# Performance work log

Hardware: AMD Instinct MI355X
Metric: run time of the kernel (lower is better)

The kernel has to match this reference:

```python
import jax, jax.numpy as jnp
import numpy as np

NODE_DIM = 512
PROMPT_DIM = 512
N_NODES = 100000
N_GRAPHS = 1024


def setup_inputs() -> dict:
    key = jax.random.key(0)
    k1, k2, k3, k4, k5, k6, k7 = jax.random.split(key, 7)
    node_feats = jax.random.normal(k1, (N_NODES, NODE_DIM), dtype=jnp.float32)
    graph_prompt = jax.random.normal(k2, (N_GRAPHS, PROMPT_DIM), dtype=jnp.float32)
    batch_idx = jnp.sort(jax.random.randint(k3, (N_NODES,), 0, N_GRAPHS))
    # Linear init ~ U(-1/sqrt(fan_in), 1/sqrt(fan_in)) like torch defaults
    fan1 = NODE_DIM + PROMPT_DIM
    b1 = 1.0 / np.sqrt(fan1)
    W1 = jax.random.uniform(k4, (fan1, NODE_DIM), minval=-b1, maxval=b1, dtype=jnp.float32)
    bias1 = jax.random.uniform(k5, (NODE_DIM,), minval=-b1, maxval=b1, dtype=jnp.float32)
    b2 = 1.0 / np.sqrt(NODE_DIM)
    W2 = jax.random.uniform(k6, (NODE_DIM, NODE_DIM), minval=-b2, maxval=b2, dtype=jnp.float32)
    bias2 = jax.random.uniform(k7, (NODE_DIM,), minval=-b2, maxval=b2, dtype=jnp.float32)
    return {"node_feats": node_feats, "graph_prompt": graph_prompt, "batch_idx": batch_idx,
            "W1": W1, "bias1": bias1, "W2": W2, "bias2": bias2}


def reference(node_feats, graph_prompt, batch_idx, W1, bias1, W2, bias2):
    # gather per-node prompt: [N, prompt_dim]
    prompt_expanded = graph_prompt[batch_idx]
    combined = jnp.concatenate([node_feats, prompt_expanded], axis=-1)  # [N, node_dim+prompt_dim]
    h = jax.nn.relu(combined @ W1 + bias1)  # [N, node_dim]
    return h @ W2 + bias2  # [N, node_dim]
```

## Files before the change

kernel.cpp:

```cpp
#include <hip/hip_runtime.h>


#define N_NODES 100000
#define NWG 3128

typedef __bf16 bf16x8 __attribute__((ext_vector_type(8)));
typedef float  f32x4  __attribute__((ext_vector_type(4)));
typedef unsigned short ushort_t;

__device__ __forceinline__ ushort_t f2bf(float f) {
  __bf16 b = (__bf16)f;
  return __builtin_bit_cast(unsigned short, b);
}

__device__ __forceinline__ bf16x8 cvt8(const float* p) {
  float4 x = *(const float4*)p;
  float4 y = *(const float4*)(p + 4);
  bf16x8 v;
  v[0] = (__bf16)x.x; v[1] = (__bf16)x.y; v[2] = (__bf16)x.z; v[3] = (__bf16)x.w;
  v[4] = (__bf16)y.x; v[5] = (__bf16)y.y; v[6] = (__bf16)y.z; v[7] = (__bf16)y.w;
  return v;
}

__device__ __forceinline__ bf16x8 cvt8v(float4 x, float4 y) {
  bf16x8 v;
  v[0] = (__bf16)x.x; v[1] = (__bf16)x.y; v[2] = (__bf16)x.z; v[3] = (__bf16)x.w;
  v[4] = (__bf16)y.x; v[5] = (__bf16)y.y; v[6] = (__bf16)y.z; v[7] = (__bf16)y.w;
  return v;
}

__device__ __forceinline__ void gload_lds16(const void* g, void* l) {
  __builtin_amdgcn_global_load_lds(
      (const __attribute__((address_space(1))) void*)g,
      (__attribute__((address_space(3))) void*)l, 16, 0, 0);
}

__global__ void prep_kernel(const float* __restrict__ W1, const float* __restrict__ W2,
                            ushort_t* __restrict__ W1T, ushort_t* __restrict__ W2T) {
  int i = blockIdx.x * 256 + threadIdx.x;
  if (i < 524288) {
    int n = i >> 10, k = i & 1023;
    W1T[i] = f2bf(W1[k * 512 + n]);
  } else if (i < 786432) {
    int j = i - 524288;
    int n = j >> 9, k = j & 511;
    W2T[j] = f2bf(W2[k * 512 + n]);
  }
}

__global__ __launch_bounds__(256, 4) void p2_kernel(
    const float* __restrict__ gp, const ushort_t* __restrict__ W1T,
    const float* __restrict__ bias1, float* __restrict__ P2) {
  const int tid = threadIdx.x, lane = tid & 63, wid = tid >> 6;
  const int lc = lane & 15, lr = lane >> 4;
  const int m0 = (blockIdx.x >> 1) * 32;
  const int col0 = (blockIdx.x & 1) * 256 + wid * 64;

  f32x4 acc[2][4];
#pragma unroll
  for (int i = 0; i < 2; ++i)
#pragma unroll
    for (int j = 0; j < 4; ++j) acc[i][j] = {0.f, 0.f, 0.f, 0.f};

  const float* a0 = gp + (size_t)(m0 + lc) * 512;
  const ushort_t* bb = W1T + (size_t)(col0 + lc) * 1024 + 512;

#pragma unroll 2
  for (int kt = 0; kt < 8; ++kt) {
    bf16x8 bfr[2][4];
#pragma unroll
    for (int kk = 0; kk < 2; ++kk)
#pragma unroll
      for (int j = 0; j < 4; ++j)
        bfr[kk][j] = *(const bf16x8*)(bb + (size_t)j * 16 * 1024 + kt * 64 + kk * 32 + lr * 8);
    bf16x8 af[2][2];
#pragma unroll
    for (int i = 0; i < 2; ++i)
#pragma unroll
      for (int kk = 0; kk < 2; ++kk)
        af[i][kk] = cvt8(a0 + (size_t)i * 16 * 512 + kt * 64 + kk * 32 + lr * 8);
#pragma unroll
    for (int kk = 0; kk < 2; ++kk)
#pragma unroll
      for (int i = 0; i < 2; ++i)
#pragma unroll
        for (int j = 0; j < 4; ++j)
          acc[i][j] = __builtin_amdgcn_mfma_f32_16x16x32_bf16(af[i][kk], bfr[kk][j], acc[i][j], 0, 0, 0);
  }

#pragma unroll
  for (int i = 0; i < 2; ++i)
#pragma unroll
    for (int r = 0; r < 4; ++r) {
      int row = m0 + i * 16 + lr * 4 + r;
#pragma unroll
      for (int j = 0; j < 4; ++j) {
        int col = col0 + j * 16 + lc;
        P2[(size_t)row * 512 + col] = acc[i][j][r] + bias1[col];
      }
    }
}

__global__ __launch_bounds__(256, 4) void g1_kernel(
    const float* __restrict__ nf, const int* __restrict__ bidx,
    const ushort_t* __restrict__ W1T, const float* __restrict__ P2,
    ushort_t* __restrict__ h) {
  __shared__ ushort_t sA[128 * 64];
  __shared__ ushort_t sB[128 * 64];

  const int tid = threadIdx.x, lane = tid & 63, wid = tid >> 6;
  const int tile = (blockIdx.x & 7) * 391 + (blockIdx.x >> 3);
  const int m0 = (tile >> 2) * 128, n0 = (tile & 3) * 128;

  const float* pAg[4]; int ldsA[4];
#pragma unroll
  for (int s = 0; s < 4; ++s) {
    int q = s * 256 + tid;
    int row = q >> 3;
    int cw = (q & 7) ^ (row & 7);
    int rowg = m0 + row; if (rowg > N_NODES - 1) rowg = N_NODES - 1;
    pAg[s] = nf + (size_t)rowg * 512 + cw * 8;
    ldsA[s] = q * 8;
  }
  const ushort_t* pB[4]; int ldsB[4];
#pragma unroll
  for (int s = 0; s < 4; ++s) {
    int q = wid * 256 + s * 64 + lane;
    int row = q >> 3;
    int cw = (q & 7) ^ (row & 7);
    pB[s] = W1T + (size_t)(n0 + row) * 1024 + cw * 8;
    ldsB[s] = (wid * 256 + s * 64) * 8;
  }

  f32x4 acc[4][4];
#pragma unroll
  for (int i = 0; i < 4; ++i)
#pragma unroll
    for (int j = 0; j < 4; ++j) acc[i][j] = {0.f, 0.f, 0.f, 0.f};

  const int wm = (wid >> 1) * 64, wn = (wid & 1) * 64;
  const int lr = lane >> 4, lc = lane & 15;

  for (int kt = 0; kt < 8; ++kt) {
    float4 ax[4], ay[4];
#pragma unroll
    for (int s = 0; s < 4; ++s) {
      ax[s] = *(const float4*)(pAg[s]);
      ay[s] = *(const float4*)(pAg[s] + 4);
      pAg[s] += 64;
    }
#pragma unroll
    for (int s = 0; s < 4; ++s) { gload_lds16(pB[s], &sB[ldsB[s]]); pB[s] += 64; }
#pragma unroll
    for (int s = 0; s < 4; ++s)
      *(bf16x8*)&sA[ldsA[s]] = cvt8v(ax[s], ay[s]);
    __syncthreads();

#pragma unroll
    for (int kk = 0; kk < 2; ++kk) {
      bf16x8 af[4], bfr[4];
#pragma unroll
      for (int i = 0; i < 4; ++i) {
        int row = wm + i * 16 + lc;
        int cp = (kk * 4 + lr) ^ (row & 7);
        af[i] = *(const bf16x8*)&sA[row * 64 + cp * 8];
      }
#pragma unroll
      for (int j = 0; j < 4; ++j) {
        int col = wn + j * 16 + lc;
        int cp = (kk * 4 + lr) ^ (col & 7);
        bfr[j] = *(const bf16x8*)&sB[col * 64 + cp * 8];
      }
#pragma unroll
      for (int i = 0; i < 4; ++i)
#pragma unroll
        for (int j = 0; j < 4; ++j)
          acc[i][j] = __builtin_amdgcn_mfma_f32_16x16x32_bf16(af[i], bfr[j], acc[i][j], 0, 0, 0);
    }
    __syncthreads();
  }

#pragma unroll
  for (int i = 0; i < 4; ++i) {
#pragma unroll
    for (int r = 0; r < 4; ++r) {
      int row = m0 + wm + i * 16 + lr * 4 + r;
      if (row < N_NODES) {
        int g = bidx[row];
        const float* p2r = P2 + (size_t)g * 512 + n0 + wn;
#pragma unroll
        for (int j = 0; j < 4; ++j) {
          float v = fmaxf(acc[i][j][r] + p2r[j * 16 + lc], 0.f);
          h[(size_t)row * 512 + n0 + wn + j * 16 + lc] = f2bf(v);
        }
      }
    }
  }
}

__global__ __launch_bounds__(256, 4) void g2_kernel(
    const ushort_t* __restrict__ h, const ushort_t* __restrict__ W2T,
    const float* __restrict__ bias2, float* __restrict__ out) {
  __shared__ ushort_t sA[128 * 64];
  __shared__ ushort_t sB[128 * 64];

  const int tid = threadIdx.x, lane = tid & 63, wid = tid >> 6;
  const int tile = (blockIdx.x & 7) * 391 + (blockIdx.x >> 3);
  const int m0 = (tile >> 2) * 128, n0 = (tile & 3) * 128;

  const ushort_t* pA[4]; const ushort_t* pB[4]; int ldsW[4];
#pragma unroll
  for (int s = 0; s < 4; ++s) {
    int q = wid * 256 + s * 64 + lane;
    int row = q >> 3;
    int cw = (q & 7) ^ (row & 7);
    int rowg = m0 + row; if (rowg > N_NODES - 1) rowg = N_NODES - 1;
    pA[s] = h + (size_t)rowg * 512 + cw * 8;
    pB[s] = W2T + (size_t)(n0 + row) * 512 + cw * 8;
    ldsW[s] = (wid * 256 + s * 64) * 8;
  }

  f32x4 acc[4][4];
#pragma unroll
  for (int i = 0; i < 4; ++i)
#pragma unroll
    for (int j = 0; j < 4; ++j) acc[i][j] = {0.f, 0.f, 0.f, 0.f};

  const int wm = (wid >> 1) * 64, wn = (wid & 1) * 64;
  const int lr = lane >> 4, lc = lane & 15;

  for (int kt = 0; kt < 8; ++kt) {
#pragma unroll
    for (int s = 0; s < 4; ++s) {
      gload_lds16(pA[s], &sA[ldsW[s]]); pA[s] += 64;
      gload_lds16(pB[s], &sB[ldsW[s]]); pB[s] += 64;
    }
    __syncthreads();
#pragma unroll
    for (int kk = 0; kk < 2; ++kk) {
      bf16x8 af[4], bfr[4];
#pragma unroll
      for (int i = 0; i < 4; ++i) {
        int row = wm + i * 16 + lc;
        int cp = (kk * 4 + lr) ^ (row & 7);
        af[i] = *(const bf16x8*)&sA[row * 64 + cp * 8];
      }
#pragma unroll
      for (int j = 0; j < 4; ++j) {
        int col = wn + j * 16 + lc;
        int cp = (kk * 4 + lr) ^ (col & 7);
        bfr[j] = *(const bf16x8*)&sB[col * 64 + cp * 8];
      }
#pragma unroll
      for (int i = 0; i < 4; ++i)
#pragma unroll
        for (int j = 0; j < 4; ++j)
          acc[i][j] = __builtin_amdgcn_mfma_f32_16x16x32_bf16(af[i], bfr[j], acc[i][j], 0, 0, 0);
    }
    __syncthreads();
  }

#pragma unroll
  for (int j = 0; j < 4; ++j) {
    int col = n0 + wn + j * 16 + lc;
    float bv = bias2[col];
#pragma unroll
    for (int i = 0; i < 4; ++i)
#pragma unroll
      for (int r = 0; r < 4; ++r) {
        int row = m0 + wm + i * 16 + lr * 4 + r;
        if (row < N_NODES) out[(size_t)row * 512 + col] = acc[i][j][r] + bv;
      }
  }
}

extern "C" void kernel_launch(void* const* d_in, const int* in_sizes, int n_in,
                              void* d_out, int out_size, void* d_ws, size_t ws_size,
                              hipStream_t stream) {
  const float* nf   = (const float*)d_in[0];
  const float* gp   = (const float*)d_in[1];
  const int*   bidx = (const int*)d_in[2];
  const float* W1   = (const float*)d_in[3];
  const float* b1   = (const float*)d_in[4];
  const float* W2   = (const float*)d_in[5];
  const float* b2   = (const float*)d_in[6];
  float* out = (float*)d_out;

  char* ws = (char*)d_ws;
  ushort_t* W1T = (ushort_t*)ws;
  ushort_t* W2T = (ushort_t*)(ws + 1048576);
  float*    P2  = (float*)   (ws + 1572864);
  ushort_t* hbf = (ushort_t*)(ws + 3670016);

  prep_kernel<<<3072, 256, 0, stream>>>(W1, W2, W1T, W2T);
  p2_kernel<<<64, 256, 0, stream>>>(gp, W1T, b1, P2);
  g1_kernel<<<NWG, 256, 0, stream>>>(nf, bidx, W1T, P2, hbf);
  g2_kernel<<<NWG, 256, 0, stream>>>(hbf, W2T, b2, out);
}
```

Baseline: 276.5 us.

## Double-buffer LDS tiles in both GEMM kernels to overlap loads with MFMA

Both GEMM kernels now use two LDS buffers for A and B. Each iteration prefetches the next K-slice into the alternate buffer while the current one is being computed, so one barrier per iteration replaces two. This should hide global-load latency behind MFMA work. In exchange, LDS use doubles to 64KB per block and the launch bound drops from 4 to 2 blocks per CU, which may reduce the occupancy-based latency hiding the kernels had before.

```diff
diff --git a/kernel.cpp b/kernel.cpp
--- a/kernel.cpp
+++ b/kernel.cpp
@@ -101,12 +101,12 @@
     }
 }
 
-__global__ __launch_bounds__(256, 4) void g1_kernel(
+__global__ __launch_bounds__(256, 2) void g1_kernel(
     const float* __restrict__ nf, const int* __restrict__ bidx,
     const ushort_t* __restrict__ W1T, const float* __restrict__ P2,
     ushort_t* __restrict__ h) {
-  __shared__ ushort_t sA[128 * 64];
-  __shared__ ushort_t sB[128 * 64];
+  __shared__ ushort_t sA[2][128 * 64];
+  __shared__ ushort_t sB[2][128 * 64];
 
   const int tid = threadIdx.x, lane = tid & 63, wid = tid >> 6;
   const int tile = (blockIdx.x & 7) * 391 + (blockIdx.x >> 3);
@@ -141,7 +141,7 @@
   const int wm = (wid >> 1) * 64, wn = (wid & 1) * 64;
   const int lr = lane >> 4, lc = lane & 15;
 
-  for (int kt = 0; kt < 8; ++kt) {
+  {
     float4 ax[4], ay[4];
 #pragma unroll
     for (int s = 0; s < 4; ++s) {
@@ -150,12 +150,28 @@
       pAg[s] += 64;
     }
 #pragma unroll
-    for (int s = 0; s < 4; ++s) { gload_lds16(pB[s], &sB[ldsB[s]]); pB[s] += 64; }
-#pragma unroll
-    for (int s = 0; s < 4; ++s)
-      *(bf16x8*)&sA[ldsA[s]] = cvt8v(ax[s], ay[s]);
+    for (int s = 0; s < 4; ++s) { gload_lds16(pB[s], &sB[0][ldsB[s]]); pB[s] += 64; }
+#pragma unroll
+    for (int s = 0; s < 4; ++s) *(bf16x8*)&sA[0][ldsA[s]] = cvt8v(ax[s], ay[s]);
     __syncthreads();
-
+  }
+
+#pragma unroll
+  for (int kt = 0; kt < 8; ++kt) {
+    const int cur = kt & 1;
+    float4 ax[4], ay[4];
+    if (kt < 7) {
+#pragma unroll
+      for (int s = 0; s < 4; ++s) {
+        ax[s] = *(const float4*)(pAg[s]);
+        ay[s] = *(const float4*)(pAg[s] + 4);
+        pAg[s] += 64;
+      }
+#pragma unroll
+      for (int s = 0; s < 4; ++s) {
+        gload_lds16(pB[s], &sB[cur ^ 1][ldsB[s]]); pB[s] += 64;
+      }
+    }
 #pragma unroll
     for (int kk = 0; kk < 2; ++kk) {
       bf16x8 af[4], bfr[4];
@@ -163,13 +179,13 @@
       for (int i = 0; i < 4; ++i) {
         int row = wm + i * 16 + lc;
         int cp = (kk * 4 + lr) ^ (row & 7);
-        af[i] = *(const bf16x8*)&sA[row * 64 + cp * 8];
+        af[i] = *(const bf16x8*)&sA[cur][row * 64 + cp * 8];
       }
 #pragma unroll
       for (int j = 0; j < 4; ++j) {
         int col = wn + j * 16 + lc;
         int cp = (kk * 4 + lr) ^ (col & 7);
-        bfr[j] = *(const bf16x8*)&sB[col * 64 + cp * 8];
+        bfr[j] = *(const bf16x8*)&sB[cur][col * 64 + cp * 8];
       }
 #pragma unroll
       for (int i = 0; i < 4; ++i)
@@ -177,7 +193,12 @@
         for (int j = 0; j < 4; ++j)
           acc[i][j] = __builtin_amdgcn_mfma_f32_16x16x32_bf16(af[i], bfr[j], acc[i][j], 0, 0, 0);
     }
-    __syncthreads();
+    if (kt < 7) {
+#pragma unroll
+      for (int s = 0; s < 4; ++s)
+        *(bf16x8*)&sA[cur ^ 1][ldsA[s]] = cvt8v(ax[s], ay[s]);
+      __syncthreads();
+    }
   }
 
 #pragma unroll
@@ -198,11 +219,11 @@
   }
 }
 
-__global__ __launch_bounds__(256, 4) void g2_kernel(
+__global__ __launch_bounds__(256, 2) void g2_kernel(
     const ushort_t* __restrict__ h, const ushort_t* __restrict__ W2T,
     const float* __restrict__ bias2, float* __restrict__ out) {
-  __shared__ ushort_t sA[128 * 64];
-  __shared__ ushort_t sB[128 * 64];
+  __shared__ ushort_t sA[2][128 * 64];
+  __shared__ ushort_t sB[2][128 * 64];
 
   const int tid = threadIdx.x, lane = tid & 63, wid = tid >> 6;
   const int tile = (blockIdx.x & 7) * 391 + (blockIdx.x >> 3);
@@ -229,13 +250,23 @@
   const int wm = (wid >> 1) * 64, wn = (wid & 1) * 64;
   const int lr = lane >> 4, lc = lane & 15;
 
+#pragma unroll
+  for (int s = 0; s < 4; ++s) {
+    gload_lds16(pA[s], &sA[0][ldsW[s]]); pA[s] += 64;
+    gload_lds16(pB[s], &sB[0][ldsW[s]]); pB[s] += 64;
+  }
+  __syncthreads();
+
+#pragma unroll
   for (int kt = 0; kt < 8; ++kt) {
-#pragma unroll
-    for (int s = 0; s < 4; ++s) {
-      gload_lds16(pA[s], &sA[ldsW[s]]); pA[s] += 64;
-      gload_lds16(pB[s], &sB[ldsW[s]]); pB[s] += 64;
-    }
-    __syncthreads();
+    const int cur = kt & 1;
+    if (kt < 7) {
+#pragma unroll
+      for (int s = 0; s < 4; ++s) {
+        gload_lds16(pA[s], &sA[cur ^ 1][ldsW[s]]); pA[s] += 64;
+        gload_lds16(pB[s], &sB[cur ^ 1][ldsW[s]]); pB[s] += 64;
+      }
+    }
 #pragma unroll
     for (int kk = 0; kk < 2; ++kk) {
       bf16x8 af[4], bfr[4];
@@ -243,13 +274,13 @@
       for (int i = 0; i < 4; ++i) {
         int row = wm + i * 16 + lc;
         int cp = (kk * 4 + lr) ^ (row & 7);
-        af[i] = *(const bf16x8*)&sA[row * 64 + cp * 8];
+        af[i] = *(const bf16x8*)&sA[cur][row * 64 + cp * 8];
       }
 #pragma unroll
       for (int j = 0; j < 4; ++j) {
         int col = wn + j * 16 + lc;
         int cp = (kk * 4 + lr) ^ (col & 7);
-        bfr[j] = *(const bf16x8*)&sB[col * 64 + cp * 8];
+        bfr[j] = *(const bf16x8*)&sB[cur][col * 64 + cp * 8];
       }
 #pragma unroll
       for (int i = 0; i < 4; ++i)
@@ -257,7 +288,7 @@
         for (int j = 0; j < 4; ++j)
           acc[i][j] = __builtin_amdgcn_mfma_f32_16x16x32_bf16(af[i], bfr[j], acc[i][j], 0, 0, 0);
     }
-    __syncthreads();
+    if (kt < 7) __syncthreads();
   }
 
 #pragma unroll
```

Measured after the change: 344.6 us. +24.6%, slower.

## Register-prefetch pipeline GEMMs, two M tiles per workgroup, XCD-contiguous tile mapping

Applied to the files above, without the earlier changes.

Both GEMM kernels now prefetch the next K slice into registers while MFMAs run on the current LDS tile. This replaces the global_load_lds DMA path with plain loads followed by LDS stores between barriers. Each workgroup processes two consecutive 128-row tiles, so the grid is halved and the prologue is amortised. A new XCD mapping keeps neighbouring tiles on the same XCD, and setprio is raised around the MFMA section. Occupancy bounds drop to 2 waves per SIMD to make room for the extra prefetch registers, at the cost of less latency hiding across workgroups.

```diff
diff --git a/kernel.cpp b/kernel.cpp
--- a/kernel.cpp
+++ b/kernel.cpp
@@ -2,7 +2,7 @@
 
 
 #define N_NODES 100000
-#define NWG 3128
+#define NWG 1564
 
 typedef __bf16 bf16x8 __attribute__((ext_vector_type(8)));
 typedef float  f32x4  __attribute__((ext_vector_type(4)));
@@ -29,10 +29,15 @@
   return v;
 }
 
-__device__ __forceinline__ void gload_lds16(const void* g, void* l) {
-  __builtin_amdgcn_global_load_lds(
-      (const __attribute__((address_space(1))) void*)g,
-      (__attribute__((address_space(3))) void*)l, 16, 0, 0);
+__device__ __forceinline__ void block_sync() {
+  __builtin_amdgcn_sched_barrier(0);
+  __builtin_amdgcn_s_barrier();
+  __builtin_amdgcn_sched_barrier(0);
+}
+
+__device__ __forceinline__ int xcd_map(int b) {
+  int xcd = b & 7, pos = b >> 3;
+  return (xcd < 4 ? xcd * 196 : 784 + (xcd - 4) * 195) + pos;
 }
 
 __global__ void prep_kernel(const float* __restrict__ W1, const float* __restrict__ W2,
@@ -101,7 +106,7 @@
     }
 }
 
-__global__ __launch_bounds__(256, 4) void g1_kernel(
+__global__ __launch_bounds__(256, 2) void g1_kernel(
     const float* __restrict__ nf, const int* __restrict__ bidx,
     const ushort_t* __restrict__ W1T, const float* __restrict__ P2,
     ushort_t* __restrict__ h) {
@@ -109,27 +114,25 @@
   __shared__ ushort_t sB[128 * 64];
 
   const int tid = threadIdx.x, lane = tid & 63, wid = tid >> 6;
-  const int tile = (blockIdx.x & 7) * 391 + (blockIdx.x >> 3);
-  const int m0 = (tile >> 2) * 128, n0 = (tile & 3) * 128;
-
-  const float* pAg[4]; int ldsA[4];
+  const int wg = xcd_map(blockIdx.x);
+  const int group = wg >> 2, nt = wg & 3;
+  const int m0 = group * 256;
+  const int n0 = nt * 128;
+
+  int arow[4], acw[4];
+  const float* pAg[4];
+  const ushort_t* pB[4];
+  int ldsQ[4];
 #pragma unroll
   for (int s = 0; s < 4; ++s) {
     int q = s * 256 + tid;
     int row = q >> 3;
     int cw = (q & 7) ^ (row & 7);
+    arow[s] = row; acw[s] = cw;
     int rowg = m0 + row; if (rowg > N_NODES - 1) rowg = N_NODES - 1;
     pAg[s] = nf + (size_t)rowg * 512 + cw * 8;
-    ldsA[s] = q * 8;
-  }
-  const ushort_t* pB[4]; int ldsB[4];
-#pragma unroll
-  for (int s = 0; s < 4; ++s) {
-    int q = wid * 256 + s * 64 + lane;
-    int row = q >> 3;
-    int cw = (q & 7) ^ (row & 7);
-    pB[s] = W1T + (size_t)(n0 + row) * 1024 + cw * 8;
-    ldsB[s] = (wid * 256 + s * 64) * 8;
+    pB[s]  = W1T + (size_t)(n0 + row) * 1024 + cw * 8;
+    ldsQ[s] = q * 8;
   }
 
   f32x4 acc[4][4];
@@ -141,21 +144,44 @@
   const int wm = (wid >> 1) * 64, wn = (wid & 1) * 64;
   const int lr = lane >> 4, lc = lane & 15;
 
-  for (int kt = 0; kt < 8; ++kt) {
-    float4 ax[4], ay[4];
+  {
+    float4 ax[4], ay[4]; int4 bv[4];
 #pragma unroll
     for (int s = 0; s < 4; ++s) {
       ax[s] = *(const float4*)(pAg[s]);
       ay[s] = *(const float4*)(pAg[s] + 4);
-      pAg[s] += 64;
-    }
-#pragma unroll
-    for (int s = 0; s < 4; ++s) { gload_lds16(pB[s], &sB[ldsB[s]]); pB[s] += 64; }
-#pragma unroll
-    for (int s = 0; s < 4; ++s)
-      *(bf16x8*)&sA[ldsA[s]] = cvt8v(ax[s], ay[s]);
+      bv[s] = *(const int4*)(pB[s]);
+      pAg[s] += 64; pB[s] += 64;
+    }
+#pragma unroll
+    for (int s = 0; s < 4; ++s) {
+      *(bf16x8*)&sA[ldsQ[s]] = cvt8v(ax[s], ay[s]);
+      *(int4*)&sB[ldsQ[s]] = bv[s];
+    }
     __syncthreads();
-
+  }
+
+  float4 ax[4], ay[4]; int4 bvr[4];
+#pragma unroll
+  for (int s = 0; s < 16; ++s) {
+    if (s < 15) {
+      if (s == 7) {
+#pragma unroll
+        for (int t = 0; t < 4; ++t) {
+          int rowg = m0 + 128 + arow[t]; if (rowg > N_NODES - 1) rowg = N_NODES - 1;
+          pAg[t] = nf + (size_t)rowg * 512 + acw[t] * 8;
+          pB[t] -= 512;
+        }
+      }
+#pragma unroll
+      for (int t = 0; t < 4; ++t) {
+        ax[t] = *(const float4*)(pAg[t]);
+        ay[t] = *(const float4*)(pAg[t] + 4);
+        bvr[t] = *(const int4*)(pB[t]);
+        pAg[t] += 64; pB[t] += 64;
+      }
+    }
+    __builtin_amdgcn_s_setprio(1);
 #pragma unroll
     for (int kk = 0; kk < 2; ++kk) {
       bf16x8 af[4], bfr[4];
@@ -177,65 +203,124 @@
         for (int j = 0; j < 4; ++j)
           acc[i][j] = __builtin_amdgcn_mfma_f32_16x16x32_bf16(af[i], bfr[j], acc[i][j], 0, 0, 0);
     }
-    __syncthreads();
-  }
-
-#pragma unroll
-  for (int i = 0; i < 4; ++i) {
-#pragma unroll
-    for (int r = 0; r < 4; ++r) {
-      int row = m0 + wm + i * 16 + lr * 4 + r;
-      if (row < N_NODES) {
-        int g = bidx[row];
-        const float* p2r = P2 + (size_t)g * 512 + n0 + wn;
-#pragma unroll
-        for (int j = 0; j < 4; ++j) {
-          float v = fmaxf(acc[i][j][r] + p2r[j * 16 + lc], 0.f);
-          h[(size_t)row * 512 + n0 + wn + j * 16 + lc] = f2bf(v);
+    __builtin_amdgcn_s_setprio(0);
+
+    if (s < 15) {
+      block_sync();
+#pragma unroll
+      for (int t = 0; t < 4; ++t) {
+        *(bf16x8*)&sA[ldsQ[t]] = cvt8v(ax[t], ay[t]);
+        *(int4*)&sB[ldsQ[t]] = bvr[t];
+      }
+      asm volatile("s_waitcnt lgkmcnt(0)" ::: "memory");
+      block_sync();
+    }
+
+    if (s == 7 || s == 15) {
+      const int m0t = m0 + (s >> 3) * 128;
+#pragma unroll
+      for (int i = 0; i < 4; ++i) {
+#pragma unroll
+        for (int r = 0; r < 4; ++r) {
+          int row = m0t + wm + i * 16 + lr * 4 + r;
+          if (row < N_NODES) {
+            int g = bidx[row];
+            const float* p2r = P2 + (size_t)g * 512 + n0 + wn;
+#pragma unroll
+            for (int j = 0; j < 4; ++j) {
+              float v = fmaxf(acc[i][j][r] + p2r[j * 16 + lc], 0.f);
+              h[(size_t)row * 512 + n0 + wn + j * 16 + lc] = f2bf(v);
+            }
+          }
         }
       }
-    }
-  }
-}
-
-__global__ __launch_bounds__(256, 4) void g2_kernel(
+      if (s == 7) {
+#pragma unroll
+        for (int i = 0; i < 4; ++i)
+#pragma unroll
+          for (int j = 0; j < 4; ++j) acc[i][j] = {0.f, 0.f, 0.f, 0.f};
+      }
+    }
+  }
+}
+
+__global__ __launch_bounds__(256, 2) void g2_kernel(
     const ushort_t* __restrict__ h, const ushort_t* __restrict__ W2T,
     const float* __restrict__ bias2, float* __restrict__ out) {
   __shared__ ushort_t sA[128 * 64];
   __shared__ ushort_t sB[128 * 64];
 
   const int tid = threadIdx.x, lane = tid & 63, wid = tid >> 6;
-  const int tile = (blockIdx.x & 7) * 391 + (blockIdx.x >> 3);
-  const int m0 = (tile >> 2) * 128, n0 = (tile & 3) * 128;
-
-  const ushort_t* pA[4]; const ushort_t* pB[4]; int ldsW[4];
+  const int wg = xcd_map(blockIdx.x);
+  const int group = wg >> 2, nt = wg & 3;
+  const int m0 = group * 256;
+  const int n0 = nt * 128;
+
+  int arow[4], acw[4];
+  const ushort_t* pA[4];
+  const ushort_t* pB[4];
+  int ldsQ[4];
 #pragma unroll
   for (int s = 0; s < 4; ++s) {
-    int q = wid * 256 + s * 64 + lane;
+    int q = s * 256 + tid;
     int row = q >> 3;
     int cw = (q & 7) ^ (row & 7);
+    arow[s] = row; acw[s] = cw;
     int rowg = m0 + row; if (rowg > N_NODES - 1) rowg = N_NODES - 1;
     pA[s] = h + (size_t)rowg * 512 + cw * 8;
     pB[s] = W2T + (size_t)(n0 + row) * 512 + cw * 8;
-    ldsW[s] = (wid * 256 + s * 64) * 8;
-  }
-
-  f32x4 acc[4][4];
-#pragma unroll
-  for (int i = 0; i < 4; ++i)
-#pragma unroll
-    for (int j = 0; j < 4; ++j) acc[i][j] = {0.f, 0.f, 0.f, 0.f};
+    ldsQ[s] = q * 8;
+  }
 
   const int wm = (wid >> 1) * 64, wn = (wid & 1) * 64;
   const int lr = lane >> 4, lc = lane & 15;
 
-  for (int kt = 0; kt < 8; ++kt) {
+  float bv2[4];
+#pragma unroll
+  for (int j = 0; j < 4; ++j) bv2[j] = bias2[n0 + wn + j * 16 + lc];
+
+  f32x4 acc[4][4];
+#pragma unroll
+  for (int i = 0; i < 4; ++i)
+#pragma unroll
+    for (int j = 0; j < 4; ++j) acc[i][j] = {0.f, 0.f, 0.f, 0.f};
+
+  {
+    int4 av[4], bv[4];
 #pragma unroll
     for (int s = 0; s < 4; ++s) {
-      gload_lds16(pA[s], &sA[ldsW[s]]); pA[s] += 64;
-      gload_lds16(pB[s], &sB[ldsW[s]]); pB[s] += 64;
+      av[s] = *(const int4*)(pA[s]);
+      bv[s] = *(const int4*)(pB[s]);
+      pA[s] += 64; pB[s] += 64;
+    }
+#pragma unroll
+    for (int s = 0; s < 4; ++s) {
+      *(int4*)&sA[ldsQ[s]] = av[s];
+      *(int4*)&sB[ldsQ[s]] = bv[s];
     }
     __syncthreads();
+  }
+
+  int4 avr[4], bvr[4];
+#pragma unroll
+  for (int s = 0; s < 16; ++s) {
+    if (s < 15) {
+      if (s == 7) {
+#pragma unroll
+        for (int t = 0; t < 4; ++t) {
+          int rowg = m0 + 128 + arow[t]; if (rowg > N_NODES - 1) rowg = N_NODES - 1;
+          pA[t] = h + (size_t)rowg * 512 + acw[t] * 8;
+          pB[t] -= 512;
+        }
+      }
+#pragma unroll
+      for (int t = 0; t < 4; ++t) {
+        avr[t] = *(const int4*)(pA[t]);
+        bvr[t] = *(const int4*)(pB[t]);
+        pA[t] += 64; pB[t] += 64;
+      }
+    }
+    __builtin_amdgcn_s_setprio(1);
 #pragma unroll
     for (int kk = 0; kk < 2; ++kk) {
       bf16x8 af[4], bfr[4];
@@ -257,20 +342,39 @@
         for (int j = 0; j < 4; ++j)
           acc[i][j] = __builtin_amdgcn_mfma_f32_16x16x32_bf16(af[i], bfr[j], acc[i][j], 0, 0, 0);
     }
-    __syncthreads();
-  }
-
-#pragma unroll
-  for (int j = 0; j < 4; ++j) {
-    int col = n0 + wn + j * 16 + lc;
-    float bv = bias2[col];
-#pragma unroll
-    for (int i = 0; i < 4; ++i)
-#pragma unroll
-      for (int r = 0; r < 4; ++r) {
-        int row = m0 + wm + i * 16 + lr * 4 + r;
-        if (row < N_NODES) out[(size_t)row * 512 + col] = acc[i][j][r] + bv;
-      }
+    __builtin_amdgcn_s_setprio(0);
+
+    if (s < 15) {
+      block_sync();
+#pragma unroll
+      for (int t = 0; t < 4; ++t) {
+        *(int4*)&sA[ldsQ[t]] = avr[t];
+        *(int4*)&sB[ldsQ[t]] = bvr[t];
+      }
+      asm volatile("s_waitcnt lgkmcnt(0)" ::: "memory");
+      block_sync();
+    }
+
+    if (s == 7 || s == 15) {
+      const int m0t = m0 + (s >> 3) * 128;
+#pragma unroll
+      for (int j = 0; j < 4; ++j) {
+        int col = n0 + wn + j * 16 + lc;
+#pragma unroll
+        for (int i = 0; i < 4; ++i)
+#pragma unroll
+          for (int r = 0; r < 4; ++r) {
+            int row = m0t + wm + i * 16 + lr * 4 + r;
+            if (row < N_NODES) out[(size_t)row * 512 + col] = acc[i][j][r] + bv2[j];
+          }
+      }
+      if (s == 7) {
+#pragma unroll
+        for (int i = 0; i < 4; ++i)
+#pragma unroll
+          for (int j = 0; j < 4; ++j) acc[i][j] = {0.f, 0.f, 0.f, 0.f};
+      }
+    }
   }
 }
 
```

Measured after the change: 589.6 us. 113% more time.

## Software-pipeline A-tile register prefetch in both GEMM kernels with manual waitcnt

Applied to the files above, without the earlier changes.

Both GEMM kernels now prefetch the next K-slice of the A operand into registers while the current slice is being consumed. In g2 the A tile moves from direct global-to-LDS loads to a register-staged path, and the loops are fully unrolled. __syncthreads is replaced by explicit s_waitcnt with partial vmcnt counts plus raw s_barrier and sched_barrier, so the next A loads stay in flight across the MFMA phase. This aims to hide global load latency behind compute, at the cost of more registers and a hand-tuned vmcnt count that must match the issued load order.

```diff
diff --git a/kernel.cpp b/kernel.cpp
--- a/kernel.cpp
+++ b/kernel.cpp
@@ -141,20 +141,34 @@
   const int wm = (wid >> 1) * 64, wn = (wid & 1) * 64;
   const int lr = lane >> 4, lc = lane & 15;
 
+  float4 ax[4], ay[4];
+#pragma unroll
+  for (int s = 0; s < 4; ++s) {
+    ax[s] = *(const float4*)(pAg[s]);
+    ay[s] = *(const float4*)(pAg[s] + 4);
+    pAg[s] += 64;
+  }
+
+#pragma unroll
   for (int kt = 0; kt < 8; ++kt) {
-    float4 ax[4], ay[4];
-#pragma unroll
-    for (int s = 0; s < 4; ++s) {
-      ax[s] = *(const float4*)(pAg[s]);
-      ay[s] = *(const float4*)(pAg[s] + 4);
-      pAg[s] += 64;
-    }
-#pragma unroll
-    for (int s = 0; s < 4; ++s) { gload_lds16(pB[s], &sB[ldsB[s]]); pB[s] += 64; }
 #pragma unroll
     for (int s = 0; s < 4; ++s)
       *(bf16x8*)&sA[ldsA[s]] = cvt8v(ax[s], ay[s]);
-    __syncthreads();
+#pragma unroll
+    for (int s = 0; s < 4; ++s) { gload_lds16(pB[s], &sB[ldsB[s]]); pB[s] += 64; }
+    if (kt < 7) {
+#pragma unroll
+      for (int s = 0; s < 4; ++s) {
+        ax[s] = *(const float4*)(pAg[s]);
+        ay[s] = *(const float4*)(pAg[s] + 4);
+        pAg[s] += 64;
+      }
+      asm volatile("s_waitcnt vmcnt(8) lgkmcnt(0)" ::: "memory");
+    } else {
+      asm volatile("s_waitcnt vmcnt(0) lgkmcnt(0)" ::: "memory");
+    }
+    __builtin_amdgcn_s_barrier();
+    __builtin_amdgcn_sched_barrier(0);
 
 #pragma unroll
     for (int kk = 0; kk < 2; ++kk) {
@@ -177,7 +191,10 @@
         for (int j = 0; j < 4; ++j)
           acc[i][j] = __builtin_amdgcn_mfma_f32_16x16x32_bf16(af[i], bfr[j], acc[i][j], 0, 0, 0);
     }
-    __syncthreads();
+    if (kt < 7) {
+      __builtin_amdgcn_s_barrier();
+      __builtin_amdgcn_sched_barrier(0);
+    }
   }
 
 #pragma unroll
@@ -208,16 +225,24 @@
   const int tile = (blockIdx.x & 7) * 391 + (blockIdx.x >> 3);
   const int m0 = (tile >> 2) * 128, n0 = (tile & 3) * 128;
 
-  const ushort_t* pA[4]; const ushort_t* pB[4]; int ldsW[4];
+  const ushort_t* pAg[4]; int ldsA[4];
+#pragma unroll
+  for (int s = 0; s < 4; ++s) {
+    int q = s * 256 + tid;
+    int row = q >> 3;
+    int cw = (q & 7) ^ (row & 7);
+    int rowg = m0 + row; if (rowg > N_NODES - 1) rowg = N_NODES - 1;
+    pAg[s] = h + (size_t)rowg * 512 + cw * 8;
+    ldsA[s] = q * 8;
+  }
+  const ushort_t* pB[4]; int ldsB[4];
 #pragma unroll
   for (int s = 0; s < 4; ++s) {
     int q = wid * 256 + s * 64 + lane;
     int row = q >> 3;
     int cw = (q & 7) ^ (row & 7);
-    int rowg = m0 + row; if (rowg > N_NODES - 1) rowg = N_NODES - 1;
-    pA[s] = h + (size_t)rowg * 512 + cw * 8;
     pB[s] = W2T + (size_t)(n0 + row) * 512 + cw * 8;
-    ldsW[s] = (wid * 256 + s * 64) * 8;
+    ldsB[s] = (wid * 256 + s * 64) * 8;
   }
 
   f32x4 acc[4][4];
@@ -229,13 +254,27 @@
   const int wm = (wid >> 1) * 64, wn = (wid & 1) * 64;
   const int lr = lane >> 4, lc = lane & 15;
 
+  int4 av[4];
+#pragma unroll
+  for (int s = 0; s < 4; ++s) { av[s] = *(const int4*)(pAg[s]); pAg[s] += 64; }
+
+#pragma unroll
   for (int kt = 0; kt < 8; ++kt) {
 #pragma unroll
-    for (int s = 0; s < 4; ++s) {
-      gload_lds16(pA[s], &sA[ldsW[s]]); pA[s] += 64;
-      gload_lds16(pB[s], &sB[ldsW[s]]); pB[s] += 64;
-    }
-    __syncthreads();
+    for (int s = 0; s < 4; ++s)
+      *(int4*)&sA[ldsA[s]] = av[s];
+#pragma unroll
+    for (int s = 0; s < 4; ++s) { gload_lds16(pB[s], &sB[ldsB[s]]); pB[s] += 64; }
+    if (kt < 7) {
+#pragma unroll
+      for (int s = 0; s < 4; ++s) { av[s] = *(const int4*)(pAg[s]); pAg[s] += 64; }
+      asm volatile("s_waitcnt vmcnt(4) lgkmcnt(0)" ::: "memory");
+    } else {
+      asm volatile("s_waitcnt vmcnt(0) lgkmcnt(0)" ::: "memory");
+    }
+    __builtin_amdgcn_s_barrier();
+    __builtin_amdgcn_sched_barrier(0);
+
 #pragma unroll
     for (int kk = 0; kk < 2; ++kk) {
       bf16x8 af[4], bfr[4];
@@ -257,7 +296,10 @@
         for (int j = 0; j < 4; ++j)
           acc[i][j] = __builtin_amdgcn_mfma_f32_16x16x32_bf16(af[i], bfr[j], acc[i][j], 0, 0, 0);
     }
-    __syncthreads();
+    if (kt < 7) {
+      __builtin_amdgcn_s_barrier();
+      __builtin_amdgcn_sched_barrier(0);
+    }
   }
 
 #pragma unroll
```

Result: slower. 377.9 us (+36.7%).
